# Kernel tuning notes

Hardware: AMD Instinct MI355X
Metric: run time of the kernel (lower is better)

## Reference

```python
import jax, jax.numpy as jnp
import numpy as np

K = 100
TEMPERATURE = 0.1


def setup_inputs() -> dict:
    key = jax.random.key(0)
    k1, k2 = jax.random.split(key)
    x = jax.random.normal(k1, (8, 128, 60, 60), dtype=jnp.float32)
    W = jax.random.normal(k2, (128, 2 * K), dtype=jnp.float32) * 0.02  # torch Linear(k*2, d_model).weight
    b = jnp.zeros((128,), dtype=jnp.float32)
    return {"x": x, "W": W, "b": b}


def reference(x, W, b):
    x0, x1 = jnp.split(x, 2, axis=0)
    n, c, h, w = x0.shape
    hw = h * w
    # n c h w -> n (h w) c
    f0 = jnp.transpose(x0.reshape(n, c, hw), (0, 2, 1))
    f1 = jnp.transpose(x1.reshape(n, c, hw), (0, 2, 1))
    # (f0/sqrt(c)) @ (f1/sqrt(c))^T / T  ==  f0 @ f1^T / (c*T)
    sm = jnp.einsum('nld,nsd->nls', f0, f1) / (c * TEMPERATURE)
    cm = (jax.nn.softmax(sm, axis=1) * jax.nn.softmax(sm, axis=2)).reshape(n, hw * hw)
    _, topi = jax.lax.top_k(cm, K)  # (n, K)
    qindex = topi // hw
    rindex = topi % hw
    coords0 = jnp.stack([qindex % w, qindex // w], axis=-1).astype(jnp.float32) / w  # (n, K, 2) as (x, y)
    coords1 = jnp.stack([rindex % w, rindex // w], axis=-1).astype(jnp.float32) / w
    # create_meshgrid(h, w, normalized=False): (1, h*w, 2) with (x, y), row-major
    gy, gx = jnp.meshgrid(jnp.arange(h), jnp.arange(w), indexing='ij')
    grid = jnp.stack([gx, gy], axis=-1).reshape(1, hw, 2).astype(jnp.float32) / w
    offsets0 = grid[:, :, None, :] - coords0[:, None, :, :]  # (n, hw, K, 2)
    offsets1 = grid[:, :, None, :] - coords1[:, None, :, :]
    emb0 = offsets0.reshape(n, hw, 2 * K) @ W.T + b  # (n, hw, d_model)
    emb1 = offsets1.reshape(n, hw, 2 * K) @ W.T + b
    f0 = f0 + emb0
    f1 = f1 + emb1
    f = jnp.concatenate([f0, f1], axis=0)  # (2n, hw, d)
    # n (h w) d -> n d h w
    return jnp.transpose(f, (0, 2, 1)).reshape(2 * n, c, h, w)
```

## Files before the change

### kernel.cpp

```cpp
#include <hip/hip_runtime.h>

#define HW 3600
#define PADR 3712
#define NF4 900
#define CAP 16384
#define KSEL 100
#define NT 58
typedef unsigned long long U64;

using short8   = __attribute__((ext_vector_type(8))) short;
using float4v  = __attribute__((ext_vector_type(4))) float;
using float16v = __attribute__((ext_vector_type(16))) float;

__device__ __forceinline__ unsigned monof(float f) {
    unsigned b = __float_as_uint(f);
    return (b & 0x80000000u) ? ~b : (b | 0x80000000u);
}
__device__ __forceinline__ float unmonof(unsigned m) {
    return __uint_as_float((m & 0x80000000u) ? (m ^ 0x80000000u) : ~m);
}
__device__ __forceinline__ unsigned short f2bf(float f) {
    unsigned b = __float_as_uint(f);
    return (unsigned short)((b + 0x7FFFu + ((b >> 16) & 1u)) >> 16);
}
__device__ __forceinline__ float bf2f(unsigned short h) {
    return __uint_as_float(((unsigned)h) << 16);
}
__device__ __forceinline__ void async16(const void* g, void* l) {
    __builtin_amdgcn_global_load_lds((const __attribute__((address_space(1))) void*)g,
                                     (__attribute__((address_space(3))) void*)l, 16, 0, 0);
}


__global__ __launch_bounds__(256) void conv_k(
    const float* __restrict__ x,
    unsigned short* __restrict__ hiT, unsigned short* __restrict__ loT,
    unsigned* __restrict__ zero_region)
{
    int b = blockIdx.z, l0 = blockIdx.x * 64, d0 = blockIdx.y * 64;
    __shared__ float t[64][65];
    int tid = threadIdx.x;
    if (blockIdx.y == 0 && blockIdx.z == 0) {
        int base = blockIdx.x * 512;
        for (int i = tid; i < 512; i += 256) {
            int g = base + i;
            if (g < 28808) zero_region[g] = 0u;
        }
    }
#pragma unroll
    for (int r = 0; r < 4; r++) {
        int idx = tid + 256 * r;
        int d = idx >> 4, lq = idx & 15;
        int l = l0 + lq * 4;
        const float* src = x + ((size_t)b * 128 + d0 + d) * HW;
        float4 v;
        if (l + 3 < HW) v = *(const float4*)(src + l);
        else {
            v.x = (l     < HW) ? src[l]     : 0.f;
            v.y = (l + 1 < HW) ? src[l + 1] : 0.f;
            v.z = (l + 2 < HW) ? src[l + 2] : 0.f;
            v.w = (l + 3 < HW) ? src[l + 3] : 0.f;
        }
        t[lq * 4 + 0][d] = v.x; t[lq * 4 + 1][d] = v.y;
        t[lq * 4 + 2][d] = v.z; t[lq * 4 + 3][d] = v.w;
    }
    __syncthreads();
    const int rblk = l0 >> 7;
#pragma unroll
    for (int r = 0; r < 2; r++) {
        int idx = tid + 256 * r;
        int l = idx & 63, dq = idx >> 6;
        unsigned hp[4], lp[4];
#pragma unroll
        for (int j = 0; j < 4; j++) {
            float f0 = t[l][dq * 8 + 2 * j], f1 = t[l][dq * 8 + 2 * j + 1];
            unsigned short h0 = f2bf(f0), h1 = f2bf(f1);
            unsigned short g0 = f2bf(f0 - bf2f(h0)), g1 = f2bf(f1 - bf2f(h1));
            hp[j] = (unsigned)h0 | ((unsigned)h1 << 16);
            lp[j] = (unsigned)g0 | ((unsigned)g1 << 16);
        }
        size_t o = ((size_t)(b * 29 + rblk) * 16 + (d0 >> 3) + dq) * 1024
                 + (size_t)((l0 + l) & 127) * 8;
        *(uint4*)(hiT + o) = make_uint4(hp[0], hp[1], hp[2], hp[3]);
        *(uint4*)(loT + o) = make_uint4(lp[0], lp[1], lp[2], lp[3]);
    }
}

__global__ __launch_bounds__(512, 4) void gemm_mfma_k(
    const unsigned short* __restrict__ hiT, const unsigned short* __restrict__ loT,
    float* __restrict__ den_row, float* __restrict__ den_col,
    float* __restrict__ maxvt)
{
    const int nwg = 29 * 29 * 4, q = nwg >> 3, r = nwg & 7;
    int orig = blockIdx.x + 29 * (blockIdx.y + 29 * blockIdx.z);
    int xcd = orig & 7, idx = orig >> 3;
    int wg = (xcd < r ? xcd * (q + 1) : r * (q + 1) + (xcd - r) * q) + idx;
    const int bx = wg % 29; int tmp = wg / 29;
    const int by = tmp % 29; const int batch = tmp / 29;

    __shared__ float T[8][1024];
    __shared__ float rsB[128];
    __shared__ float csB[128];
    __shared__ unsigned mxB[2][128];

    const int tid = threadIdx.x;
    const int lane = tid & 63, w = tid >> 6;
    const int l31 = lane & 31, h = lane >> 5;
    const int rg = w >> 2, cg = w & 3;

    if (tid < 128) { rsB[tid] = 0.f; csB[tid] = 0.f; }
    if (tid < 256) mxB[tid >> 7][tid & 127] = 0u;

    const size_t cbaseA = ((size_t)(batch * 29 + by) * 16) * 1024;
    const size_t cbaseB = ((size_t)((batch + 4) * 29 + bx) * 16) * 1024;
    const unsigned short* Ah = hiT + cbaseA + (size_t)h * 1024 + (size_t)(rg * 64 + l31) * 8;
    const unsigned short* Al = loT + cbaseA + (size_t)h * 1024 + (size_t)(rg * 64 + l31) * 8;
    const unsigned short* Bh = hiT + cbaseB + (size_t)h * 1024 + (size_t)(cg * 32 + l31) * 8;
    const unsigned short* Bl = loT + cbaseB + (size_t)h * 1024 + (size_t)(cg * 32 + l31) * 8;

    float16v acc[2];
    acc[0] = (float16v)(0.f);
    acc[1] = (float16v)(0.f);

#pragma unroll
    for (int ks = 0; ks < 4; ks++) {
        short8 fah[2][2], fal[2][2], fbh[2], fbl[2];
#pragma unroll
        for (int j = 0; j < 2; j++) {
            const size_t off = (size_t)(ks * 4 + j * 2) * 1024;
            fah[j][0] = *(const short8*)(Ah + off);
            fah[j][1] = *(const short8*)(Ah + off + 256);
            fal[j][0] = *(const short8*)(Al + off);
            fal[j][1] = *(const short8*)(Al + off + 256);
            fbh[j]    = *(const short8*)(Bh + off);
            fbl[j]    = *(const short8*)(Bl + off);
        }
#pragma unroll
        for (int j = 0; j < 2; j++) {
#pragma unroll
            for (int mt = 0; mt < 2; mt++) {
                acc[mt] = __builtin_amdgcn_mfma_f32_32x32x16_bf16(fah[j][mt], fbh[j], acc[mt], 0, 0, 0);
                acc[mt] = __builtin_amdgcn_mfma_f32_32x32x16_bf16(fah[j][mt], fbl[j], acc[mt], 0, 0, 0);
                acc[mt] = __builtin_amdgcn_mfma_f32_32x32x16_bf16(fal[j][mt], fbh[j], acc[mt], 0, 0, 0);
            }
        }
    }
    __syncthreads();

    const float scale = 0.078125f;
    float* Tw = &T[w][0];
    const bool interior = (bx < 28) && (by < 28);
    const int col0 = bx * 128 + cg * 32 + l31;
    const bool cv = interior || (col0 < HW);
    float cs = 0.f;

#pragma unroll
    for (int mt = 0; mt < 2; mt++) {
#pragma unroll
        for (int reg = 0; reg < 16; reg++) {
            float v = acc[mt][reg] * scale;
            float e = cv ? __expf(v) : 0.f;
            int rloc = (reg & 3) + 8 * (reg >> 2) + 4 * h;
            bool rv = interior || (by * 128 + rg * 64 + mt * 32 + rloc < HW);
            if (rv) cs += e;
            Tw[rloc * 32 + (l31 ^ rloc)] = e;
        }
        __asm__ __volatile__("s_waitcnt lgkmcnt(0)" ::: "memory");
        {
            float ps = 0.f, pm = 0.f;
#pragma unroll
            for (int i = 0; i < 16; i++) {
                float tv_ = Tw[l31 * 32 + ((h * 16 + i) ^ l31)];
                ps += tv_;
                pm = fmaxf(pm, tv_);
            }
            ps += __shfl_xor(ps, 32);
            pm = fmaxf(pm, __shfl_xor(pm, 32));
            if (h == 0) {
                atomicAdd(&rsB[rg * 64 + mt * 32 + l31], ps);
                atomicMax(&mxB[cg >> 1][rg * 64 + mt * 32 + l31],
                          monof(__logf(pm)));
            }
        }
        __asm__ __volatile__("s_waitcnt lgkmcnt(0)" ::: "memory");
    }
    cs += __shfl_xor(cs, 32);
    if (h == 0) atomicAdd(&csB[cg * 32 + l31], cs);
    __syncthreads();

    if (tid < 128) {
        int l = by * 128 + tid;
        if (l < HW) atomicAdd(&den_row[(size_t)batch * HW + l], rsB[tid]);
        int s = bx * 128 + tid;
        if (s < HW) atomicAdd(&den_col[(size_t)batch * HW + s], csB[tid]);
    }
    if (tid < 256) {
        int tile = tid >> 7, row = tid & 127;
        int l = by * 128 + row;
        if (l < HW)
            maxvt[((size_t)batch * NT + bx * 2 + tile) * PADR + l] =
                unmonof(mxB[tile][row]);
    }
}

__global__ __launch_bounds__(256) void stat_k(
    const float* __restrict__ den_row, const float* __restrict__ den_col,
    const float* __restrict__ maxvt, float* __restrict__ keylb)
{
    const int b = blockIdx.z, tid = threadIdx.x;
    __shared__ float lncS[HW];
    __shared__ float mlsS[NT];
    for (int i = tid; i < HW; i += 256)
        lncS[i] = __logf(den_col[(size_t)b * HW + i]);
    __syncthreads();
    if (tid < NT) {
        float mx = -3.4e38f;
        int s0 = tid * 64, s1 = s0 + 64; if (s1 > HW) s1 = HW;
        for (int s = s0; s < s1; s++) mx = fmaxf(mx, lncS[s]);
        mlsS[tid] = (s0 < HW) ? mx : 1e30f;
    }
    __syncthreads();
    int j = blockIdx.x * 240 + tid;
    if (tid < 240 && j < HW) {
        const float* mvb = maxvt + (size_t)b * NT * PADR;
        float b0 = -3.4e38f, b1_ = -3.4e38f;
#pragma unroll 4
        for (int tt = 0; tt < 58; tt += 2) {
            b0  = fmaxf(b0,  2.0f * mvb[(size_t)tt * PADR + j]       - mlsS[tt]);
            b1_ = fmaxf(b1_, 2.0f * mvb[(size_t)(tt + 1) * PADR + j] - mlsS[tt + 1]);
        }
        keylb[(size_t)b * HW + j] = fmaxf(b0, b1_) - __logf(den_row[(size_t)b * HW + j]);
    }
}

__global__ __launch_bounds__(256) void tau_k(
    const float* __restrict__ keylb, float* __restrict__ tau)
{
    const int b = blockIdx.z, tid = threadIdx.x;
    __shared__ unsigned keyS[HW];
    __shared__ unsigned hist[4096];
    __shared__ unsigned hpc[256];
    __shared__ int b1S, c1S, b2S, lcnt;
    __shared__ unsigned bestS;
    __shared__ unsigned list[1024];

    for (int i = tid; i < 4096; i += 256) hist[i] = 0u;
    if (tid == 0) { lcnt = 0; bestS = 0u; }
    __syncthreads();
    for (int i = tid; i < HW; i += 256) {
        unsigned k = monof(keylb[(size_t)b * HW + i]);
        keyS[i] = k;
        atomicAdd(&hist[k >> 20], 1u);
    }
    __syncthreads();
    { unsigned s = 0; for (int j = 0; j < 16; j++) s += hist[tid * 16 + j]; hpc[tid] = s; }
    __syncthreads();
    if (tid == 0) {
        unsigned cum = 0; int cs_ = 255;
        for (; cs_ > 0; cs_--) { if (cum + hpc[cs_] >= (unsigned)KSEL) break; cum += hpc[cs_]; }
        int bb = cs_ * 16 + 15;
        for (; bb > cs_ * 16; bb--) { if (cum + hist[bb] >= (unsigned)KSEL) break; cum += hist[bb]; }
        b1S = bb; c1S = (int)cum;
    }
    __syncthreads();
    int b1 = b1S;
    for (int i = tid; i < 4096; i += 256) hist[i] = 0u;
    __syncthreads();
    for (int i = tid; i < HW; i += 256) {
        unsigned k = keyS[i];
        if ((int)(k >> 20) == b1) atomicAdd(&hist[(k >> 8) & 4095], 1u);
    }
    __syncthreads();
    { unsigned s = 0; for (int j = 0; j < 16; j++) s += hist[tid * 16 + j]; hpc[tid] = s; }
    __syncthreads();
    if (tid == 0) {
        unsigned cum = (unsigned)c1S; int cs_ = 255;
        for (; cs_ > 0; cs_--) { if (cum + hpc[cs_] >= (unsigned)KSEL) break; cum += hpc[cs_]; }
        int bb = cs_ * 16 + 15;
        for (; bb > cs_ * 16; bb--) { if (cum + hist[bb] >= (unsigned)KSEL) break; cum += hist[bb]; }
        b2S = bb;
    }
    __syncthreads();
    int b2 = b2S;
    for (int i = tid; i < HW; i += 256) {
        unsigned k = keyS[i]; int hb = (int)(k >> 20);
        if (hb > b1 || (hb == b1 && (int)((k >> 8) & 4095) >= b2)) {
            int p = atomicAdd(&lcnt, 1);
            if (p < 1024) list[p] = k;
        }
    }
    __syncthreads();
    int L = lcnt; if (L > 1024) L = 1024;
    for (int i = tid; i < L; i += 256) {
        unsigned e = list[i]; int c = 0;
        for (int j = 0; j < L; j++) c += (list[j] >= e) ? 1 : 0;
        if (c >= KSEL) atomicMax(&bestS, e);
    }
    __syncthreads();
    if (tid == 0) tau[b] = unmonof(bestS) - 3e-4f;
}

__global__ __launch_bounds__(256) void recollect_k(
    const unsigned short* __restrict__ hiT, const unsigned short* __restrict__ loT,
    const float* __restrict__ den_row, const float* __restrict__ den_col,
    const float* __restrict__ maxvt, const float* __restrict__ tau,
    uint2* __restrict__ cand, int* __restrict__ cnt)
{
    const int t = blockIdx.x, batch = blockIdx.y & 3, s = blockIdx.y >> 2;
    const int r0 = s * 900;
    const int tid = threadIdx.x;
    __shared__ float lnrS[900];
    __shared__ float lncS[64];
    __shared__ int prS[1024];
    __shared__ int pcS;
    __shared__ float mnlS;
    __shared__ __align__(16) unsigned short bS[2][16][64][8];

    const int lane = tid & 63, w = tid >> 6;
    const size_t bbase = (size_t)(batch + 4) * PADR * 128;

    {
        const size_t sbase = bbase + (size_t)(t >> 1) * 16 * 1024
                           + (size_t)(t & 1) * 512 + (size_t)lane * 8;
#pragma unroll
        for (int sl = w; sl < 32; sl += 4) {
            const int buf = sl >> 4, kb = sl & 15;
            const unsigned short* g = (buf ? loT : hiT) + sbase + (size_t)kb * 1024;
            async16(g, &bS[buf][kb][0][0]);
        }
    }

    if (tid < 64) {
        int c = t * 64 + tid;
        float lc = (c < HW) ? __logf(den_col[(size_t)batch * HW + c]) : 1e30f;
        lncS[tid] = lc;
        float mn = lc;
#pragma unroll
        for (int off = 1; off < 64; off <<= 1) mn = fminf(mn, __shfl_xor(mn, off));
        if (tid == 0) mnlS = mn;
    }
    for (int r = tid; r < 900; r += 256)
        lnrS[r] = __logf(den_row[(size_t)batch * HW + r0 + r]);
    if (tid == 0) pcS = 0;
    __syncthreads();

    const float tv = tau[batch];
    const float tvm = tv - 3e-4f;
    const float mnl = mnlS;
    const float* mv = maxvt + ((size_t)batch * NT + t) * PADR;
    for (int r = tid; r < 900; r += 256) {
        int rr = r0 + r;
        float bnd = 2.0f * mv[rr] - lnrS[r] - mnl;
        if (bnd >= tvm) {
            int p = atomicAdd(&pcS, 1);
            if (p < 1024) prS[p] = rr;
        }
    }
    __syncthreads();
    int pc = pcS; if (pc > 1024) pc = 1024;
    if (pc == 0) return;

    const int m = lane & 15, q = lane >> 4;
    const float scale = 0.078125f;
    const size_t abase = (size_t)batch * PADR * 128;

    for (int g = w; g * 16 < pc; g += 4) {
        int pi = g * 16 + m;
        int rowv = (pi < pc) ? prS[pi] : HW;
        float ldrv = (pi < pc) ? lnrS[rowv - r0] : 0.f;
        size_t arow = abase + ((size_t)(rowv >> 7) * 16) * 1024 + (size_t)(rowv & 127) * 8;

        float4v acc[4];
#pragma unroll
        for (int i = 0; i < 4; i++) acc[i] = (float4v){0.f, 0.f, 0.f, 0.f};
#pragma unroll
        for (int k0 = 0; k0 < 128; k0 += 32) {
            int kb = (k0 >> 3) + q;
            short8 ah = *(const short8*)(hiT + arow + (size_t)kb * 1024);
            short8 al = *(const short8*)(loT + arow + (size_t)kb * 1024);
#pragma unroll
            for (int nt = 0; nt < 4; nt++) {
                short8 bh = *(const short8*)&bS[0][kb][nt * 16 + m][0];
                short8 bl = *(const short8*)&bS[1][kb][nt * 16 + m][0];
                acc[nt] = __builtin_amdgcn_mfma_f32_16x16x32_bf16(ah, bh, acc[nt], 0, 0, 0);
                acc[nt] = __builtin_amdgcn_mfma_f32_16x16x32_bf16(ah, bl, acc[nt], 0, 0, 0);
                acc[nt] = __builtin_amdgcn_mfma_f32_16x16x32_bf16(al, bh, acc[nt], 0, 0, 0);
            }
        }
#pragma unroll
        for (int nt = 0; nt < 4; nt++) {
            int c = t * 64 + nt * 16 + m;
            if (c >= HW) continue;
            float ldc = lncS[nt * 16 + m];
#pragma unroll
            for (int r = 0; r < 4; r++) {
                int ri = q * 4 + r;
                if (g * 16 + ri >= pc) continue;
                int rowo = __shfl(rowv, ri);
                float ldro = __shfl(ldrv, ri);
                float v = acc[nt][r] * scale;
                float tt2 = 2.0f * v - ldro - ldc;
                if (tt2 >= tv) {
                    int p = atomicAdd(&cnt[batch], 1);
                    if (p < CAP)
                        cand[(size_t)batch * CAP + p] =
                            make_uint2(monof(tt2), (unsigned)(rowo * HW + c));
                }
            }
        }
    }
}

__global__ __launch_bounds__(1024) void select_k(
    const uint2* __restrict__ cand, const int* __restrict__ cnt,
    const float* __restrict__ W, const float* __restrict__ bias,
    float* __restrict__ cst, float* __restrict__ sxy)
{
    const int batch = blockIdx.x;
    const int tid = threadIdx.x;
    const uint2* cb = cand + (size_t)batch * CAP;
    __shared__ unsigned hist[4096];
    __shared__ unsigned hpc[256];
    __shared__ int b1S, c1S, b2S, lcnt;
    __shared__ U64 list[1024];
    __shared__ int topiS[KSEL];
    __shared__ float cqx[KSEL], cqy[KSEL], crx[KSEL], cry[KSEL];

    int M = cnt[batch]; if (M > CAP) M = CAP;
    for (int i = tid; i < 4096; i += 1024) hist[i] = 0u;
    if (tid == 0) lcnt = 0;
    __syncthreads();
    for (int i = tid; i < M; i += 1024) atomicAdd(&hist[cb[i].x >> 20], 1u);
    __syncthreads();
    if (tid < 256) { unsigned s = 0; for (int j = 0; j < 16; j++) s += hist[tid * 16 + j]; hpc[tid] = s; }
    __syncthreads();
    if (tid == 0) {
        unsigned cum = 0; int cs_ = 255;
        for (; cs_ > 0; cs_--) { if (cum + hpc[cs_] >= (unsigned)KSEL) break; cum += hpc[cs_]; }
        int bb = cs_ * 16 + 15;
        for (; bb > cs_ * 16; bb--) { if (cum + hist[bb] >= (unsigned)KSEL) break; cum += hist[bb]; }
        b1S = bb; c1S = (int)cum;
    }
    __syncthreads();
    const int b1 = b1S;
    for (int i = tid; i < 4096; i += 1024) hist[i] = 0u;
    __syncthreads();
    for (int i = tid; i < M; i += 1024) {
        unsigned x = cb[i].x;
        if ((int)(x >> 20) == b1) atomicAdd(&hist[(x >> 8) & 4095], 1u);
    }
    __syncthreads();
    if (tid < 256) { unsigned s = 0; for (int j = 0; j < 16; j++) s += hist[tid * 16 + j]; hpc[tid] = s; }
    __syncthreads();
    if (tid == 0) {
        unsigned cum = (unsigned)c1S; int cs_ = 255;
        for (; cs_ > 0; cs_--) { if (cum + hpc[cs_] >= (unsigned)KSEL) break; cum += hpc[cs_]; }
        int bb = cs_ * 16 + 15;
        for (; bb > cs_ * 16; bb--) { if (cum + hist[bb] >= (unsigned)KSEL) break; cum += hist[bb]; }
        b2S = bb;
    }
    __syncthreads();
    const int b2 = b2S;
    for (int i = tid; i < M; i += 1024) {
        uint2 e = cb[i];
        int hb = (int)(e.x >> 20);
        if (hb > b1 || (hb == b1 && (int)((e.x >> 8) & 4095) >= b2)) {
            int p = atomicAdd(&lcnt, 1);
            if (p < 1024) list[p] = ((U64)e.x << 32) | (unsigned)(~e.y);
        }
    }
    __syncthreads();
    int L = lcnt; if (L > 1024) L = 1024;
    for (int i = tid; i < L; i += 1024) {
        U64 e = list[i]; int r = 0;
        for (int j = 0; j < L; j++) r += (list[j] > e) ? 1 : 0;
        if (r < KSEL) topiS[r] = (int)(~(unsigned)(e & 0xffffffffu));
    }
    __syncthreads();
    if (tid < KSEL) {
        int idx = topiS[tid];
        int qq = idx / HW, rr = idx - qq * HW;
        cqx[tid] = (float)(qq % 60) / 60.0f;
        cqy[tid] = (float)(qq / 60) / 60.0f;
        crx[tid] = (float)(rr % 60) / 60.0f;
        cry[tid] = (float)(rr / 60) / 60.0f;
    }
    __syncthreads();
    if (tid < 256) {
        const int d = tid & 127, hf = tid >> 7;
        const float* wrow = W + d * 200;
        float sx = 0.f, sy = 0.f, c = 0.f;
#pragma unroll 4
        for (int k = 0; k < KSEL; k++) {
            float wx = wrow[2 * k], wy = wrow[2 * k + 1];
            sx += wx; sy += wy;
            float cx = hf ? crx[k] : cqx[k];
            float cy = hf ? cry[k] : cqy[k];
            c += cx * wx + cy * wy;
        }
        cst[(hf ? (batch + 4) : batch) * 128 + d] = bias[d] - c;
        if (batch == 0 && hf == 0) { sxy[d] = sx; sxy[128 + d] = sy; }
    }
}

__global__ __launch_bounds__(256) void final_k(
    const float* __restrict__ x, const float* __restrict__ cst,
    const float* __restrict__ sxy, float* __restrict__ out)
{
    const int bd = blockIdx.x;
    const int d = bd & 127;
    const int tid = threadIdx.x;
    const float cstv = cst[bd];
    const float sx = sxy[d], sy = sxy[128 + d];
    const float4* xin = (const float4*)(x + (size_t)bd * HW);
    float4* o4 = (float4*)(out + (size_t)bd * HW);
    for (int f = tid; f < NF4; f += 256) {
        float4 v = xin[f];
        int p0 = f * 4;
        float gy = (float)(p0 / 60) / 60.0f;
        float gxb = (float)(p0 % 60);
        float add = cstv + gy * sy;
        v.x += add + ((gxb      ) / 60.0f) * sx;
        v.y += add + ((gxb + 1.f) / 60.0f) * sx;
        v.z += add + ((gxb + 2.f) / 60.0f) * sx;
        v.w += add + ((gxb + 3.f) / 60.0f) * sx;
        o4[f] = v;
    }
}

extern "C" void kernel_launch(void* const* d_in, const int* in_sizes, int n_in,
                              void* d_out, int out_size, void* d_ws, size_t ws_size,
                              hipStream_t stream)
{
    const float* x    = (const float*)d_in[0];
    const float* W    = (const float*)d_in[1];
    const float* bias = (const float*)d_in[2];
    float* out = (float*)d_out;

    char* ws = (char*)d_ws;
    float*    den_row = (float*)(ws + 0);
    float*    den_col = (float*)(ws + 57600);
    int*      cnt     = (int*)  (ws + 115200);
    float*    tau     = (float*)(ws + 115216);
    float*    keylb   = (float*)(ws + 115264);
    float*    cst     = (float*)(ws + 115264);
    float*    sxy     = (float*)(ws + 119360);
    uint2*    cand    = (uint2*)(ws + 172864);
    float*    maxvt   = (float*)(ws + 697152);
    unsigned short* hiT = (unsigned short*)(ws + 4141888);
    unsigned short* loT = (unsigned short*)(ws + 11744064);

    conv_k     <<<dim3(58, 2, 8),  256, 0, stream>>>(x, hiT, loT, (unsigned*)ws);
    gemm_mfma_k<<<dim3(29, 29, 4), 512, 0, stream>>>(hiT, loT, den_row, den_col, maxvt);
    stat_k     <<<dim3(15, 1, 4),  256, 0, stream>>>(den_row, den_col, maxvt, keylb);
    tau_k      <<<dim3(1, 1, 4),   256, 0, stream>>>(keylb, tau);
    recollect_k<<<dim3(NT, 16),    256, 0, stream>>>(hiT, loT, den_row, den_col, maxvt, tau, cand, cnt);
    select_k   <<<dim3(4),         1024, 0, stream>>>(cand, cnt, W, bias, cst, sxy);
    final_k    <<<dim3(1024),      256, 0, stream>>>(x, cst, sxy, out);
}
```

Baseline: 226.7 us.

## Fuse stat/tau kernels and fold top-k selection into final output kernel

Merges the key lower-bound computation and threshold selection into a single per-batch 1024-thread kernel, eliminating the keylb round trip and one launch. Moves the candidate top-k selection and positional-embedding constant computation into each block of the final elementwise kernel, removing the select launch and the cst/sxy buffers. This trades launch overhead and serial small-grid stages for redundant per-block selection work and reduced parallelism in the stat stage.

```diff
diff --git a/kernel.cpp b/kernel.cpp
--- a/kernel.cpp
+++ b/kernel.cpp
@@ -203,40 +203,13 @@
     }
 }
 
-__global__ __launch_bounds__(256) void stat_k(
+__global__ __launch_bounds__(1024) void stattau_k(
     const float* __restrict__ den_row, const float* __restrict__ den_col,
-    const float* __restrict__ maxvt, float* __restrict__ keylb)
+    const float* __restrict__ maxvt, float* __restrict__ tau)
 {
-    const int b = blockIdx.z, tid = threadIdx.x;
+    const int b = blockIdx.x, tid = threadIdx.x;
     __shared__ float lncS[HW];
     __shared__ float mlsS[NT];
-    for (int i = tid; i < HW; i += 256)
-        lncS[i] = __logf(den_col[(size_t)b * HW + i]);
-    __syncthreads();
-    if (tid < NT) {
-        float mx = -3.4e38f;
-        int s0 = tid * 64, s1 = s0 + 64; if (s1 > HW) s1 = HW;
-        for (int s = s0; s < s1; s++) mx = fmaxf(mx, lncS[s]);
-        mlsS[tid] = (s0 < HW) ? mx : 1e30f;
-    }
-    __syncthreads();
-    int j = blockIdx.x * 240 + tid;
-    if (tid < 240 && j < HW) {
-        const float* mvb = maxvt + (size_t)b * NT * PADR;
-        float b0 = -3.4e38f, b1_ = -3.4e38f;
-#pragma unroll 4
-        for (int tt = 0; tt < 58; tt += 2) {
-            b0  = fmaxf(b0,  2.0f * mvb[(size_t)tt * PADR + j]       - mlsS[tt]);
-            b1_ = fmaxf(b1_, 2.0f * mvb[(size_t)(tt + 1) * PADR + j] - mlsS[tt + 1]);
-        }
-        keylb[(size_t)b * HW + j] = fmaxf(b0, b1_) - __logf(den_row[(size_t)b * HW + j]);
-    }
-}
-
-__global__ __launch_bounds__(256) void tau_k(
-    const float* __restrict__ keylb, float* __restrict__ tau)
-{
-    const int b = blockIdx.z, tid = threadIdx.x;
     __shared__ unsigned keyS[HW];
     __shared__ unsigned hist[4096];
     __shared__ unsigned hpc[256];
@@ -244,16 +217,34 @@
     __shared__ unsigned bestS;
     __shared__ unsigned list[1024];
 
-    for (int i = tid; i < 4096; i += 256) hist[i] = 0u;
+    for (int i = tid; i < HW; i += 1024)
+        lncS[i] = __logf(den_col[(size_t)b * HW + i]);
+    for (int i = tid; i < 4096; i += 1024) hist[i] = 0u;
     if (tid == 0) { lcnt = 0; bestS = 0u; }
     __syncthreads();
-    for (int i = tid; i < HW; i += 256) {
-        unsigned k = monof(keylb[(size_t)b * HW + i]);
-        keyS[i] = k;
-        atomicAdd(&hist[k >> 20], 1u);
-    }
-    __syncthreads();
-    { unsigned s = 0; for (int j = 0; j < 16; j++) s += hist[tid * 16 + j]; hpc[tid] = s; }
+    if (tid < NT) {
+        float mx = -3.4e38f;
+        int s0 = tid * 64, s1 = s0 + 64; if (s1 > HW) s1 = HW;
+        for (int s = s0; s < s1; s++) mx = fmaxf(mx, lncS[s]);
+        mlsS[tid] = (s0 < HW) ? mx : 1e30f;
+    }
+    __syncthreads();
+    {
+        const float* mvb = maxvt + (size_t)b * NT * PADR;
+        for (int j = tid; j < HW; j += 1024) {
+            float b0 = -3.4e38f, b1_ = -3.4e38f;
+#pragma unroll 4
+            for (int tt = 0; tt < 58; tt += 2) {
+                b0  = fmaxf(b0,  2.0f * mvb[(size_t)tt * PADR + j]       - mlsS[tt]);
+                b1_ = fmaxf(b1_, 2.0f * mvb[(size_t)(tt + 1) * PADR + j] - mlsS[tt + 1]);
+            }
+            unsigned k = monof(fmaxf(b0, b1_) - __logf(den_row[(size_t)b * HW + j]));
+            keyS[j] = k;
+            atomicAdd(&hist[k >> 20], 1u);
+        }
+    }
+    __syncthreads();
+    if (tid < 256) { unsigned s = 0; for (int j = 0; j < 16; j++) s += hist[tid * 16 + j]; hpc[tid] = s; }
     __syncthreads();
     if (tid == 0) {
         unsigned cum = 0; int cs_ = 255;
@@ -264,14 +255,14 @@
     }
     __syncthreads();
     int b1 = b1S;
-    for (int i = tid; i < 4096; i += 256) hist[i] = 0u;
-    __syncthreads();
-    for (int i = tid; i < HW; i += 256) {
+    for (int i = tid; i < 4096; i += 1024) hist[i] = 0u;
+    __syncthreads();
+    for (int i = tid; i < HW; i += 1024) {
         unsigned k = keyS[i];
         if ((int)(k >> 20) == b1) atomicAdd(&hist[(k >> 8) & 4095], 1u);
     }
     __syncthreads();
-    { unsigned s = 0; for (int j = 0; j < 16; j++) s += hist[tid * 16 + j]; hpc[tid] = s; }
+    if (tid < 256) { unsigned s = 0; for (int j = 0; j < 16; j++) s += hist[tid * 16 + j]; hpc[tid] = s; }
     __syncthreads();
     if (tid == 0) {
         unsigned cum = (unsigned)c1S; int cs_ = 255;
@@ -282,7 +273,7 @@
     }
     __syncthreads();
     int b2 = b2S;
-    for (int i = tid; i < HW; i += 256) {
+    for (int i = tid; i < HW; i += 1024) {
         unsigned k = keyS[i]; int hb = (int)(k >> 20);
         if (hb > b1 || (hb == b1 && (int)((k >> 8) & 4095) >= b2)) {
             int p = atomicAdd(&lcnt, 1);
@@ -291,7 +282,7 @@
     }
     __syncthreads();
     int L = lcnt; if (L > 1024) L = 1024;
-    for (int i = tid; i < L; i += 256) {
+    for (int i = tid; i < L; i += 1024) {
         unsigned e = list[i]; int c = 0;
         for (int j = 0; j < L; j++) c += (list[j] >= e) ? 1 : 0;
         if (c >= KSEL) atomicMax(&bestS, e);
@@ -411,28 +402,36 @@
     }
 }
 
-__global__ __launch_bounds__(1024) void select_k(
+__global__ __launch_bounds__(256) void final_k(
+    const float* __restrict__ x, const float* __restrict__ W,
+    const float* __restrict__ bias,
     const uint2* __restrict__ cand, const int* __restrict__ cnt,
-    const float* __restrict__ W, const float* __restrict__ bias,
-    float* __restrict__ cst, float* __restrict__ sxy)
+    float* __restrict__ out)
 {
-    const int batch = blockIdx.x;
+    const int bd = blockIdx.x;
+    const int b8 = bd >> 7, d = bd & 127;
+    const int batch = b8 & 3;
+    const bool useQ = (b8 < 4);
     const int tid = threadIdx.x;
+    const int lane = tid & 63, w = tid >> 6;
     const uint2* cb = cand + (size_t)batch * CAP;
+
     __shared__ unsigned hist[4096];
     __shared__ unsigned hpc[256];
     __shared__ int b1S, c1S, b2S, lcnt;
     __shared__ U64 list[1024];
     __shared__ int topiS[KSEL];
-    __shared__ float cqx[KSEL], cqy[KSEL], crx[KSEL], cry[KSEL];
+    __shared__ float cxS[KSEL], cyS[KSEL];
+    __shared__ float redC[4], redX[4], redY[4];
+    __shared__ float cstS, sxS, syS;
 
     int M = cnt[batch]; if (M > CAP) M = CAP;
-    for (int i = tid; i < 4096; i += 1024) hist[i] = 0u;
+    for (int i = tid; i < 4096; i += 256) hist[i] = 0u;
     if (tid == 0) lcnt = 0;
     __syncthreads();
-    for (int i = tid; i < M; i += 1024) atomicAdd(&hist[cb[i].x >> 20], 1u);
-    __syncthreads();
-    if (tid < 256) { unsigned s = 0; for (int j = 0; j < 16; j++) s += hist[tid * 16 + j]; hpc[tid] = s; }
+    for (int i = tid; i < M; i += 256) atomicAdd(&hist[cb[i].x >> 20], 1u);
+    __syncthreads();
+    { unsigned s = 0; for (int j = 0; j < 16; j++) s += hist[tid * 16 + j]; hpc[tid] = s; }
     __syncthreads();
     if (tid == 0) {
         unsigned cum = 0; int cs_ = 255;
@@ -443,14 +442,14 @@
     }
     __syncthreads();
     const int b1 = b1S;
-    for (int i = tid; i < 4096; i += 1024) hist[i] = 0u;
-    __syncthreads();
-    for (int i = tid; i < M; i += 1024) {
-        unsigned x = cb[i].x;
-        if ((int)(x >> 20) == b1) atomicAdd(&hist[(x >> 8) & 4095], 1u);
-    }
-    __syncthreads();
-    if (tid < 256) { unsigned s = 0; for (int j = 0; j < 16; j++) s += hist[tid * 16 + j]; hpc[tid] = s; }
+    for (int i = tid; i < 4096; i += 256) hist[i] = 0u;
+    __syncthreads();
+    for (int i = tid; i < M; i += 256) {
+        unsigned xk = cb[i].x;
+        if ((int)(xk >> 20) == b1) atomicAdd(&hist[(xk >> 8) & 4095], 1u);
+    }
+    __syncthreads();
+    { unsigned s = 0; for (int j = 0; j < 16; j++) s += hist[tid * 16 + j]; hpc[tid] = s; }
     __syncthreads();
     if (tid == 0) {
         unsigned cum = (unsigned)c1S; int cs_ = 255;
@@ -461,7 +460,7 @@
     }
     __syncthreads();
     const int b2 = b2S;
-    for (int i = tid; i < M; i += 1024) {
+    for (int i = tid; i < M; i += 256) {
         uint2 e = cb[i];
         int hb = (int)(e.x >> 20);
         if (hb > b1 || (hb == b1 && (int)((e.x >> 8) & 4095) >= b2)) {
@@ -471,7 +470,7 @@
     }
     __syncthreads();
     int L = lcnt; if (L > 1024) L = 1024;
-    for (int i = tid; i < L; i += 1024) {
+    for (int i = tid; i < L; i += 256) {
         U64 e = list[i]; int r = 0;
         for (int j = 0; j < L; j++) r += (list[j] > e) ? 1 : 0;
         if (r < KSEL) topiS[r] = (int)(~(unsigned)(e & 0xffffffffu));
@@ -480,38 +479,32 @@
     if (tid < KSEL) {
         int idx = topiS[tid];
         int qq = idx / HW, rr = idx - qq * HW;
-        cqx[tid] = (float)(qq % 60) / 60.0f;
-        cqy[tid] = (float)(qq / 60) / 60.0f;
-        crx[tid] = (float)(rr % 60) / 60.0f;
-        cry[tid] = (float)(rr / 60) / 60.0f;
-    }
-    __syncthreads();
-    if (tid < 256) {
-        const int d = tid & 127, hf = tid >> 7;
-        const float* wrow = W + d * 200;
-        float sx = 0.f, sy = 0.f, c = 0.f;
-#pragma unroll 4
-        for (int k = 0; k < KSEL; k++) {
-            float wx = wrow[2 * k], wy = wrow[2 * k + 1];
-            sx += wx; sy += wy;
-            float cx = hf ? crx[k] : cqx[k];
-            float cy = hf ? cry[k] : cqy[k];
-            c += cx * wx + cy * wy;
-        }
-        cst[(hf ? (batch + 4) : batch) * 128 + d] = bias[d] - c;
-        if (batch == 0 && hf == 0) { sxy[d] = sx; sxy[128 + d] = sy; }
-    }
-}
-
-__global__ __launch_bounds__(256) void final_k(
-    const float* __restrict__ x, const float* __restrict__ cst,
-    const float* __restrict__ sxy, float* __restrict__ out)
-{
-    const int bd = blockIdx.x;
-    const int d = bd & 127;
-    const int tid = threadIdx.x;
-    const float cstv = cst[bd];
-    const float sx = sxy[d], sy = sxy[128 + d];
+        int sel = useQ ? qq : rr;
+        cxS[tid] = (float)(sel % 60) / 60.0f;
+        cyS[tid] = (float)(sel / 60) / 60.0f;
+    }
+    __syncthreads();
+    float pC = 0.f, pX = 0.f, pY = 0.f;
+    if (tid < KSEL) {
+        float wx = W[d * 200 + 2 * tid], wy = W[d * 200 + 2 * tid + 1];
+        pC = cxS[tid] * wx + cyS[tid] * wy;
+        pX = wx; pY = wy;
+    }
+#pragma unroll
+    for (int off = 1; off < 64; off <<= 1) {
+        pC += __shfl_xor(pC, off);
+        pX += __shfl_xor(pX, off);
+        pY += __shfl_xor(pY, off);
+    }
+    if (lane == 0) { redC[w] = pC; redX[w] = pX; redY[w] = pY; }
+    __syncthreads();
+    if (tid == 0) {
+        cstS = bias[d] - (redC[0] + redC[1] + redC[2] + redC[3]);
+        sxS  = redX[0] + redX[1] + redX[2] + redX[3];
+        syS  = redY[0] + redY[1] + redY[2] + redY[3];
+    }
+    __syncthreads();
+    const float cst = cstS, sx = sxS, sy = syS;
     const float4* xin = (const float4*)(x + (size_t)bd * HW);
     float4* o4 = (float4*)(out + (size_t)bd * HW);
     for (int f = tid; f < NF4; f += 256) {
@@ -519,8 +512,8 @@
         int p0 = f * 4;
         float gy = (float)(p0 / 60) / 60.0f;
         float gxb = (float)(p0 % 60);
-        float add = cstv + gy * sy;
-        v.x += add + ((gxb      ) / 60.0f) * sx;
+        float add = cst + gy * sy;
+        v.x += add + ((gxb       ) / 60.0f) * sx;
         v.y += add + ((gxb + 1.f) / 60.0f) * sx;
         v.z += add + ((gxb + 2.f) / 60.0f) * sx;
         v.w += add + ((gxb + 3.f) / 60.0f) * sx;
@@ -542,19 +535,14 @@
     float*    den_col = (float*)(ws + 57600);
     int*      cnt     = (int*)  (ws + 115200);
     float*    tau     = (float*)(ws + 115216);
-    float*    keylb   = (float*)(ws + 115264);
-    float*    cst     = (float*)(ws + 115264);
-    float*    sxy     = (float*)(ws + 119360);
     uint2*    cand    = (uint2*)(ws + 172864);
     float*    maxvt   = (float*)(ws + 697152);
     unsigned short* hiT = (unsigned short*)(ws + 4141888);
     unsigned short* loT = (unsigned short*)(ws + 11744064);
 
-    conv_k     <<<dim3(58, 2, 8),  256, 0, stream>>>(x, hiT, loT, (unsigned*)ws);
-    gemm_mfma_k<<<dim3(29, 29, 4), 512, 0, stream>>>(hiT, loT, den_row, den_col, maxvt);
-    stat_k     <<<dim3(15, 1, 4),  256, 0, stream>>>(den_row, den_col, maxvt, keylb);
-    tau_k      <<<dim3(1, 1, 4),   256, 0, stream>>>(keylb, tau);
-    recollect_k<<<dim3(NT, 16),    256, 0, stream>>>(hiT, loT, den_row, den_col, maxvt, tau, cand, cnt);
-    select_k   <<<dim3(4),         1024, 0, stream>>>(cand, cnt, W, bias, cst, sxy);
-    final_k    <<<dim3(1024),      256, 0, stream>>>(x, cst, sxy, out);
-}
+    conv_k     <<<dim3(58, 2, 8),  256,  0, stream>>>(x, hiT, loT, (unsigned*)ws);
+    gemm_mfma_k<<<dim3(29, 29, 4), 512,  0, stream>>>(hiT, loT, den_row, den_col, maxvt);
+    stattau_k  <<<dim3(4),         1024, 0, stream>>>(den_row, den_col, maxvt, tau);
+    recollect_k<<<dim3(NT, 16),    256,  0, stream>>>(hiT, loT, den_row, den_col, maxvt, tau, cand, cnt);
+    final_k    <<<dim3(1024),      256,  0, stream>>>(x, W, bias, cand, cnt, out);
+}
```

Measured after the change: 221.4 us. 1.02x faster.
